# Kernel tuning notes

Hardware: AMD Instinct MI355X
Metric: run time of the kernel (lower is better)

Reference implementation:

```python
import jax, jax.numpy as jnp
import numpy as np

B, D, H, HD, P, O, K = 256, 1024, 8, 128, 2048, 1024, 4
HID = H * HD
EPS = 1e-5


def setup_inputs() -> dict:
    key = jax.random.key(0)
    ks = jax.random.split(key, 16)

    def w(k, shape, fan_in):
        return jax.random.normal(k, shape, jnp.float32) / np.sqrt(fan_in).astype(np.float32)

    return dict(
        seq=jax.random.normal(ks[0], (B, D), jnp.float32),
        c_tm1=jnp.zeros((B, H, HD, HD), jnp.float32),
        n_tm1=jnp.ones((B, H, HD), jnp.float32),
        m_tm1=jnp.zeros((B, H), jnp.float32),
        ln_g=jnp.ones((D,), jnp.float32), ln_b=jnp.zeros((D,), jnp.float32),
        gn_g=jnp.ones((HID,), jnp.float32), gn_b=jnp.zeros((HID,), jnp.float32),
        W_upl=w(ks[1], (P, D), D), b_upl=jnp.zeros((P,), jnp.float32),
        W_upr=w(ks[2], (HID, D), D), b_upr=jnp.zeros((HID,), jnp.float32),
        W_down=w(ks[3], (D, HID), HID), b_down=jnp.zeros((D,), jnp.float32),
        W_last=w(ks[4], (O, D), D), b_last=jnp.zeros((O,), jnp.float32),
        conv_w=w(ks[5], (K,), K), conv_b=jnp.zeros((), jnp.float32),
        W_skip=w(ks[6], (HID, P), P),
        W_i=w(ks[7], (H, P), P), b_i=jnp.zeros((H,), jnp.float32),
        W_f=w(ks[8], (H, P), P), b_f=jnp.zeros((H,), jnp.float32),
        W_o=w(ks[9], (HID, P), P), b_o=jnp.zeros((HID,), jnp.float32),
        W_q=w(ks[10], (HID, P), P), b_q=jnp.zeros((HID,), jnp.float32),
        W_k=w(ks[11], (HID, P), P), b_k=jnp.zeros((HID,), jnp.float32),
        W_v=w(ks[12], (HID, P), P), b_v=jnp.zeros((HID,), jnp.float32),
    )


def reference(seq, c_tm1, n_tm1, m_tm1, ln_g, ln_b, gn_g, gn_b,
              W_upl, b_upl, W_upr, b_upr, W_down, b_down, W_last, b_last,
              conv_w, conv_b, W_skip, W_i, b_i, W_f, b_f, W_o, b_o,
              W_q, b_q, W_k, b_k, W_v, b_v):
    b = seq.shape[0]
    h, hd = c_tm1.shape[1], c_tm1.shape[2]

    # input LayerNorm
    mu = jnp.mean(seq, -1, keepdims=True)
    var = jnp.var(seq, -1, keepdims=True)
    x_n = (seq - mu) * jax.lax.rsqrt(var + EPS) * ln_g + ln_b

    x_t = x_n @ W_upl.T + b_upl            # [b, P]
    r_t = x_n @ W_upr.T + b_upr            # [b, HID]

    # causal conv over the feature axis (in=out=1 channel), left pad K-1
    k_sz = conv_w.shape[0]
    p = x_t.shape[1]
    xp = jnp.pad(x_t, ((0, 0), (k_sz - 1, 0)))
    x_c = conv_b + sum(conv_w[j] * xp[:, j:j + p] for j in range(k_sz))
    x_c = jax.nn.silu(x_c)                 # [b, P]

    q_t = (x_c @ W_q.T + b_q).reshape(b, h, hd)
    k_t = ((x_c @ W_k.T + b_k) / np.sqrt(hd).astype(np.float32)).reshape(b, h, hd)
    v_t = (x_t @ W_v.T + b_v).reshape(b, h, hd)

    i_t = x_c @ W_i.T + b_i                # [b, h]
    f_t = x_c @ W_f.T + b_f                # [b, h]
    o_t = jax.nn.sigmoid(x_t @ W_o.T + b_o)  # [b, HID]

    # stabilized exponential gating
    m_t = jnp.maximum(f_t + m_tm1, i_t)
    i_g = jnp.exp(i_t - m_t)
    f_g = jnp.exp(f_t - m_t + m_tm1)

    # matrix-memory covariance update
    c_t = f_g[:, :, None, None] * c_tm1 + i_g[:, :, None, None] * jnp.einsum('bhd,bhp->bhdp', v_t, k_t)
    n_t = f_g[:, :, None] * n_tm1 + i_g[:, :, None] * k_t

    num = jnp.einsum('bhdp,bhp->bhd', c_t, q_t)
    den = jnp.maximum(jnp.einsum('bhd,bhd->bh', n_t, q_t), 1.0)
    h_t = o_t * (num / den[:, :, None]).reshape(b, h * hd)

    # GroupNorm(head_num groups) over hidden
    hg = h_t.reshape(b, h, hd)
    gmu = jnp.mean(hg, -1, keepdims=True)
    gvar = jnp.var(hg, -1, keepdims=True)
    hn = ((hg - gmu) * jax.lax.rsqrt(gvar + EPS)).reshape(b, h * hd) * gn_g + gn_b

    out = hn + x_c @ W_skip.T              # 1x1 conv skip == matmul
    out = out * jax.nn.silu(r_t)
    out = out @ W_down.T + b_down
    final = (out + x_n) @ W_last.T + b_last
    return final, c_t, n_t, m_t
```

## Files before the change

### kernel.cpp

```cpp
#include <hip/hip_runtime.h>
#include <cstdint>
#include <cstddef>

#define LN_EPS 1e-5f

typedef float  f32x4  __attribute__((ext_vector_type(4)));
typedef __bf16 bf16x8 __attribute__((ext_vector_type(8)));
typedef unsigned short u16x4 __attribute__((ext_vector_type(4)));

__global__ __launch_bounds__(256)
void k_ln(const float* __restrict__ seq, const float* __restrict__ g,
          const float* __restrict__ b, float* __restrict__ xn) {
  __shared__ float red[8];
  const int row = blockIdx.x, t = threadIdx.x;
  const f32x4 x = ((const f32x4*)(seq + (size_t)row * 1024))[t];
  float s  = x[0] + x[1] + x[2] + x[3];
  float s2 = x[0]*x[0] + x[1]*x[1] + x[2]*x[2] + x[3]*x[3];
#pragma unroll
  for (int o = 32; o > 0; o >>= 1) { s += __shfl_down(s, o, 64); s2 += __shfl_down(s2, o, 64); }
  const int lane = t & 63, w = t >> 6;
  if (lane == 0) { red[w] = s; red[4 + w] = s2; }
  __syncthreads();
  s  = red[0] + red[1] + red[2] + red[3];
  s2 = red[4] + red[5] + red[6] + red[7];
  const float mu  = s * (1.f / 1024.f);
  const float inv = rsqrtf(s2 * (1.f / 1024.f) - mu * mu + LN_EPS);
  const f32x4 gg = ((const f32x4*)g)[t];
  const f32x4 bb = ((const f32x4*)b)[t];
  f32x4 y;
#pragma unroll
  for (int i = 0; i < 4; ++i) y[i] = (x[i] - mu) * inv * gg[i] + bb[i];
  ((f32x4*)(xn + (size_t)row * 1024))[t] = y;
}

__global__ __launch_bounds__(256)
void k_conv(const float* __restrict__ xt, const float* __restrict__ cw,
            const float* __restrict__ cb, float* __restrict__ xc) {
  __shared__ float s[2048];
  const int row = blockIdx.x, t = threadIdx.x;
  const f32x4* src = (const f32x4*)(xt + (size_t)row * 2048);
  ((f32x4*)s)[t] = src[t];
  ((f32x4*)s)[t + 256] = src[t + 256];
  const float w0 = cw[0], w1 = cw[1], w2 = cw[2], w3 = cw[3], b = cb[0];
  __syncthreads();
  float out[8];
  const int c0 = t * 8;
#pragma unroll
  for (int j = 0; j < 8; ++j) {
    const int c = c0 + j;
    float a = b + w3 * s[c];
    if (c >= 1) a += w2 * s[c - 1];
    if (c >= 2) a += w1 * s[c - 2];
    if (c >= 3) a += w0 * s[c - 3];
    a = a / (1.f + __expf(-a));
    out[j] = a;
  }
  f32x4* dst = (f32x4*)(xc + (size_t)row * 2048 + c0);
  f32x4 v0 = {out[0], out[1], out[2], out[3]};
  f32x4 v1 = {out[4], out[5], out[6], out[7]};
  dst[0] = v0; dst[1] = v1;
}

__global__ __launch_bounds__(256)
void k_if(const float* __restrict__ xc, const float* __restrict__ Wi,
          const float* __restrict__ bi, const float* __restrict__ Wf,
          const float* __restrict__ bfp, const float* __restrict__ m_tm1,
          float* __restrict__ m_out, float* __restrict__ ig, float* __restrict__ fg) {
  __shared__ float sx[2048];
  __shared__ float so[16];
  const int row = blockIdx.x, t = threadIdx.x;
  const f32x4* src = (const f32x4*)(xc + (size_t)row * 2048);
  ((f32x4*)sx)[t] = src[t];
  ((f32x4*)sx)[t + 256] = src[t + 256];
  __syncthreads();
  const int w = t >> 6, lane = t & 63;
  float p[4];
#pragma unroll
  for (int i = 0; i < 4; ++i) {
    const int o = w * 4 + i;
    const float* wr = (o < 8) ? (Wi + (size_t)o * 2048) : (Wf + (size_t)(o - 8) * 2048);
    float acc = 0.f;
#pragma unroll
    for (int j = 0; j < 8; ++j) {
      const f32x4 xv = ((const f32x4*)sx)[j * 64 + lane];
      const f32x4 wv = ((const f32x4*)wr)[j * 64 + lane];
      acc += xv[0]*wv[0] + xv[1]*wv[1] + xv[2]*wv[2] + xv[3]*wv[3];
    }
    p[i] = acc;
  }
#pragma unroll
  for (int i = 0; i < 4; ++i) {
#pragma unroll
    for (int o = 32; o > 0; o >>= 1) p[i] += __shfl_xor(p[i], o, 64);
  }
  if (lane == 0) {
#pragma unroll
    for (int i = 0; i < 4; ++i) so[w * 4 + i] = p[i];
  }
  __syncthreads();
  if (t < 8) {
    const float it = so[t] + bi[t];
    const float ft = so[t + 8] + bfp[t];
    const float mp = m_tm1[row * 8 + t];
    const float m = fmaxf(ft + mp, it);
    m_out[row * 8 + t] = m;
    ig[row * 8 + t] = __expf(it - m);
    fg[row * 8 + t] = __expf(ft - m + mp);
  }
}

__global__ __launch_bounds__(256)
void k_rec_stream(const float* __restrict__ c_tm1, const float* __restrict__ kb,
                  const float* __restrict__ qb, const float* __restrict__ vb,
                  const float* __restrict__ ig, const float* __restrict__ fg,
                  float* __restrict__ c_out, float* __restrict__ numG) {
  const int blk = blockIdx.x;
  const int bh = blk >> 2;
  const int rg = blk & 3;
  const int t = threadIdx.x;
  const int w = t >> 6, lane = t & 63;
  const int c4 = lane & 31;
  const int half = lane >> 5;
  const int b = bh >> 3, h = bh & 7;
  const size_t vecbase = (size_t)b * 1024 + h * 128;
  const float fgv = fg[bh], igv = ig[bh];
  const f32x4 k4 = ((const f32x4*)(kb + vecbase))[c4];
  const f32x4 q4 = ((const f32x4*)(qb + vecbase))[c4];
  const int row0 = rg * 32 + w * 8;
  const f32x4* C0 = (const f32x4*)(c_tm1 + (size_t)bh * 16384);
  f32x4* Ct = (f32x4*)(c_out + (size_t)bh * 16384);
  f32x4 c0s[4]; float vrow[4];
#pragma unroll
  for (int j = 0; j < 4; ++j) {
    const int r = row0 + 2 * j + half;
    c0s[j] = C0[r * 32 + c4];
    vrow[j] = vb[vecbase + r];
  }
#pragma unroll
  for (int j = 0; j < 4; ++j)
    asm volatile("" : "+v"(c0s[j][0]), "+v"(c0s[j][1]), "+v"(c0s[j][2]), "+v"(c0s[j][3]));
  float pd[4];
#pragma unroll
  for (int j = 0; j < 4; ++j) {
    const int r = row0 + 2 * j + half;
    const float iv = igv * vrow[j];
    f32x4 ct = fgv * c0s[j] + iv * k4;
    Ct[r * 32 + c4] = ct;
    pd[j] = ct[0] * q4[0] + ct[1] * q4[1] + ct[2] * q4[2] + ct[3] * q4[3];
  }
#pragma unroll
  for (int j = 0; j < 4; ++j) {
    float p = pd[j];
    p += __shfl_xor(p, 1, 64); p += __shfl_xor(p, 2, 64); p += __shfl_xor(p, 4, 64);
    p += __shfl_xor(p, 8, 64); p += __shfl_xor(p, 16, 64);
    if (c4 == 0) numG[(size_t)bh * 128 + row0 + 2 * j + half] = p;
  }
}

__device__ __forceinline__ float bsum128(float v, volatile float* red) {
#pragma unroll
  for (int o = 32; o > 0; o >>= 1) v += __shfl_xor(v, o, 64);
  const int w = threadIdx.x >> 6;
  __syncthreads();
  if ((threadIdx.x & 63) == 0) red[w] = v;
  __syncthreads();
  return red[0] + red[1];
}

__global__ __launch_bounds__(128)
void k_rec_fin(const float* __restrict__ n_tm1, const float* __restrict__ kb,
               const float* __restrict__ qb, const float* __restrict__ ot,
               const float* __restrict__ ig, const float* __restrict__ fg,
               const float* __restrict__ numG,
               const float* __restrict__ gn_g, const float* __restrict__ gn_b,
               const float* __restrict__ skipb, const float* __restrict__ sr,
               float* __restrict__ n_out, float* __restrict__ uf) {
  __shared__ float red[2];
  const int bh = blockIdx.x, t = threadIdx.x;
  const int b = bh >> 3, h = bh & 7;
  const size_t base = (size_t)b * 1024 + h * 128;
  const float fgv = fg[bh], igv = ig[bh];
  const float ntd = fgv * n_tm1[(size_t)bh * 128 + t] + igv * kb[base + t];
  n_out[(size_t)bh * 128 + t] = ntd;
  const float den = fmaxf(bsum128(ntd * qb[base + t], red), 1.f);
  const float o = 1.f / (1.f + __expf(-ot[base + t]));
  const float hv = o * numG[(size_t)bh * 128 + t] / den;
  const float mu  = bsum128(hv, red) * (1.f / 128.f);
  const float var = bsum128(hv * hv, red) * (1.f / 128.f) - mu * mu;
  const int hid = h * 128 + t;
  const float hn = (hv - mu) * rsqrtf(var + LN_EPS) * gn_g[hid] + gn_b[hid];
  uf[base + t] = (hn + skipb[base + t]) * sr[base + t];
}

struct GemmSeg {
  const float* A; const float* W; const float* bias; float* out;
  const float* add; int ldOut; int colOfs; int epi; float scale;
};
struct GemmArgs { GemmSeg seg[5]; };

__global__ __launch_bounds__(256)
void k_gemm(int K, GemmArgs ga) {
  __shared__ __align__(16) char lds[32768];
  const int tid = threadIdx.x;
  const int lane = tid & 63;
  const int wid = tid >> 6;
  const int wm = wid >> 1;
  const int wn = wid & 1;
  const int segId = blockIdx.x >> 4;
  const int n0 = (blockIdx.x & 15) * 64;
  const int m0 = blockIdx.y * 64;
  const GemmSeg sg = ga.seg[segId];

  const int lrow = tid >> 4;
  const int col4 = tid & 15;

  f32x4 acc[2][2] = {};

  const float* Abase = sg.A + (size_t)m0 * K;
  const float* Wbase = sg.W + (size_t)n0 * K;
  const int NT = K >> 6;

  f32x4 va[4], vw[4], va2[4], vw2[4];
#pragma unroll
  for (int p = 0; p < 4; ++p) {
    const int r = p * 16 + lrow;
    va[p] = *(const f32x4*)(Abase + (size_t)r * K + col4 * 4);
    vw[p] = *(const f32x4*)(Wbase + (size_t)r * K + col4 * 4);
  }

  for (int kt = 0; kt < NT; ++kt) {
    __syncthreads();
    {
      const int byte = ((((col4 >> 1) ^ (lrow & 7)) << 4) | ((col4 & 1) << 3));
#pragma unroll
      for (int p = 0; p < 4; ++p) {
        const int r = p * 16 + lrow;
        u16x4 ah, al, wh, wl;
#pragma unroll
        for (int i = 0; i < 4; ++i) {
          const unsigned ab = __float_as_uint(va[p][i]);
          const float fh = __uint_as_float(ab & 0xFFFF0000u);
          ah[i] = (unsigned short)(ab >> 16);
          al[i] = (unsigned short)(__float_as_uint(va[p][i] - fh) >> 16);
          const unsigned wb2 = __float_as_uint(vw[p][i]);
          const float wfh = __uint_as_float(wb2 & 0xFFFF0000u);
          wh[i] = (unsigned short)(wb2 >> 16);
          wl[i] = (unsigned short)(__float_as_uint(vw[p][i] - wfh) >> 16);
        }
        *(u16x4*)(lds + r * 128 + byte) = ah;
        *(u16x4*)(lds + 8192 + r * 128 + byte) = al;
        *(u16x4*)(lds + 16384 + r * 128 + byte) = wh;
        *(u16x4*)(lds + 24576 + r * 128 + byte) = wl;
      }
    }
    if (kt + 1 < NT) {
      const int ko = (kt + 1) * 64;
#pragma unroll
      for (int p = 0; p < 4; ++p) {
        const int r = p * 16 + lrow;
        va2[p] = *(const f32x4*)(Abase + (size_t)r * K + ko + col4 * 4);
        vw2[p] = *(const f32x4*)(Wbase + (size_t)r * K + ko + col4 * 4);
      }
    }
    __syncthreads();
    {
      const int rA = wm * 32 + (lane & 15);
      const int rB = wn * 32 + (lane & 15);
      const int kg = lane >> 4;
      const int swz = lane & 7;
#pragma unroll
      for (int kk = 0; kk < 2; ++kk) {
        const int so = ((kk * 4 + kg) ^ swz) << 4;
        const char* pa0 = lds + rA * 128 + so;
        const char* pa1 = lds + (rA + 16) * 128 + so;
        const char* pb0 = lds + 16384 + rB * 128 + so;
        const char* pb1 = lds + 16384 + (rB + 16) * 128 + so;
        const bf16x8 ah0 = *(const bf16x8*)(pa0);
        const bf16x8 al0 = *(const bf16x8*)(pa0 + 8192);
        const bf16x8 ah1 = *(const bf16x8*)(pa1);
        const bf16x8 al1 = *(const bf16x8*)(pa1 + 8192);
        const bf16x8 bh0 = *(const bf16x8*)(pb0);
        const bf16x8 bl0 = *(const bf16x8*)(pb0 + 8192);
        const bf16x8 bh1 = *(const bf16x8*)(pb1);
        const bf16x8 bl1 = *(const bf16x8*)(pb1 + 8192);
        acc[0][0] = __builtin_amdgcn_mfma_f32_16x16x32_bf16(ah0, bh0, acc[0][0], 0, 0, 0);
        acc[0][1] = __builtin_amdgcn_mfma_f32_16x16x32_bf16(ah0, bh1, acc[0][1], 0, 0, 0);
        acc[1][0] = __builtin_amdgcn_mfma_f32_16x16x32_bf16(ah1, bh0, acc[1][0], 0, 0, 0);
        acc[1][1] = __builtin_amdgcn_mfma_f32_16x16x32_bf16(ah1, bh1, acc[1][1], 0, 0, 0);
        acc[0][0] = __builtin_amdgcn_mfma_f32_16x16x32_bf16(ah0, bl0, acc[0][0], 0, 0, 0);
        acc[0][1] = __builtin_amdgcn_mfma_f32_16x16x32_bf16(ah0, bl1, acc[0][1], 0, 0, 0);
        acc[1][0] = __builtin_amdgcn_mfma_f32_16x16x32_bf16(ah1, bl0, acc[1][0], 0, 0, 0);
        acc[1][1] = __builtin_amdgcn_mfma_f32_16x16x32_bf16(ah1, bl1, acc[1][1], 0, 0, 0);
        acc[0][0] = __builtin_amdgcn_mfma_f32_16x16x32_bf16(al0, bh0, acc[0][0], 0, 0, 0);
        acc[0][1] = __builtin_amdgcn_mfma_f32_16x16x32_bf16(al0, bh1, acc[0][1], 0, 0, 0);
        acc[1][0] = __builtin_amdgcn_mfma_f32_16x16x32_bf16(al1, bh0, acc[1][0], 0, 0, 0);
        acc[1][1] = __builtin_amdgcn_mfma_f32_16x16x32_bf16(al1, bh1, acc[1][1], 0, 0, 0);
      }
    }
#pragma unroll
    for (int p = 0; p < 4; ++p) { va[p] = va2[p]; vw[p] = vw2[p]; }
  }

  const int rowb = m0 + wm * 32 + (lane >> 4) * 4;
  const int colb = n0 + wn * 32 + (lane & 15);
#pragma unroll
  for (int mf = 0; mf < 2; ++mf) {
#pragma unroll
    for (int nf = 0; nf < 2; ++nf) {
      const int col = colb + nf * 16;
      const float bv = sg.bias ? sg.bias[col] : 0.f;
#pragma unroll
      for (int i = 0; i < 4; ++i) {
        const int row = rowb + mf * 16 + i;
        float v = acc[mf][nf][i] + bv;
        if (sg.epi == 1)      v = v / (1.f + __expf(-v));
        else if (sg.epi == 3) v *= sg.scale;
        else if (sg.epi == 4) v += sg.add[(size_t)row * 1024 + col];
        sg.out[(size_t)row * sg.ldOut + sg.colOfs + col] = v;
      }
    }
  }
}

extern "C" void kernel_launch(void* const* d_in, const int* in_sizes, int n_in,
                              void* d_out, int out_size, void* d_ws, size_t ws_size,
                              hipStream_t stream) {
  (void)in_sizes; (void)n_in; (void)out_size; (void)ws_size;
  const float* seq    = (const float*)d_in[0];
  const float* c_tm1  = (const float*)d_in[1];
  const float* n_tm1  = (const float*)d_in[2];
  const float* m_tm1  = (const float*)d_in[3];
  const float* ln_g   = (const float*)d_in[4];
  const float* ln_b   = (const float*)d_in[5];
  const float* gn_g   = (const float*)d_in[6];
  const float* gn_b   = (const float*)d_in[7];
  const float* W_upl  = (const float*)d_in[8];
  const float* b_upl  = (const float*)d_in[9];
  const float* W_upr  = (const float*)d_in[10];
  const float* b_upr  = (const float*)d_in[11];
  const float* W_down = (const float*)d_in[12];
  const float* b_down = (const float*)d_in[13];
  const float* W_last = (const float*)d_in[14];
  const float* b_last = (const float*)d_in[15];
  const float* conv_w = (const float*)d_in[16];
  const float* conv_b = (const float*)d_in[17];
  const float* W_skip = (const float*)d_in[18];
  const float* W_i    = (const float*)d_in[19];
  const float* b_i    = (const float*)d_in[20];
  const float* W_f    = (const float*)d_in[21];
  const float* b_f    = (const float*)d_in[22];
  const float* W_o    = (const float*)d_in[23];
  const float* b_o    = (const float*)d_in[24];
  const float* W_q    = (const float*)d_in[25];
  const float* b_q    = (const float*)d_in[26];
  const float* W_k    = (const float*)d_in[27];
  const float* b_k    = (const float*)d_in[28];
  const float* W_v    = (const float*)d_in[29];
  const float* b_v    = (const float*)d_in[30];

  float* out_final = (float*)d_out;
  float* out_c = out_final + (size_t)256 * 1024;
  float* out_n = out_c + (size_t)256 * 8 * 128 * 128;
  float* out_m = out_n + (size_t)256 * 8 * 128;

  char* ws = (char*)d_ws;
  size_t off = 0;
  auto alloc = [&](size_t bytes) -> void* {
    void* p = ws + off; off += (bytes + 255) & ~(size_t)255; return p;
  };
  float* x_n   = (float*)alloc((size_t)256 * 1024 * 4);
  float* x_t   = (float*)alloc((size_t)256 * 2048 * 4);
  float* sr    = (float*)alloc((size_t)256 * 1024 * 4);
  float* x_c   = (float*)alloc((size_t)256 * 2048 * 4);
  float* qb    = (float*)alloc((size_t)256 * 1024 * 4);
  float* kb    = (float*)alloc((size_t)256 * 1024 * 4);
  float* vb    = (float*)alloc((size_t)256 * 1024 * 4);
  float* otb   = (float*)alloc((size_t)256 * 1024 * 4);
  float* skipb = (float*)alloc((size_t)256 * 1024 * 4);
  float* igb   = (float*)alloc((size_t)2048 * 4);
  float* fgb   = (float*)alloc((size_t)2048 * 4);
  float* u_f   = (float*)alloc((size_t)256 * 1024 * 4);
  float* t_f   = (float*)alloc((size_t)256 * 1024 * 4);
  float* numG  = (float*)alloc((size_t)2048 * 128 * 4);

  k_ln<<<256, 256, 0, stream>>>(seq, ln_g, ln_b, x_n);

  GemmArgs gA = {};
  gA.seg[0] = {x_n, W_upl, b_upl, x_t, nullptr, 2048, 0, 0, 0.f};
  gA.seg[1] = {x_n, W_upl + (size_t)1024 * 1024, b_upl + 1024, x_t, nullptr, 2048, 1024, 0, 0.f};
  gA.seg[2] = {x_n, W_upr, b_upr, sr, nullptr, 1024, 0, 1, 0.f};
  k_gemm<<<dim3(48, 4), 256, 0, stream>>>(1024, gA);

  k_conv<<<256, 256, 0, stream>>>(x_t, conv_w, conv_b, x_c);

  k_if<<<256, 256, 0, stream>>>(x_c, W_i, b_i, W_f, b_f, m_tm1, out_m, igb, fgb);

  GemmArgs gBC = {};
  gBC.seg[0] = {x_c, W_q, b_q, qb, nullptr, 1024, 0, 0, 0.f};
  gBC.seg[1] = {x_c, W_k, b_k, kb, nullptr, 1024, 0, 3, 0.08838834764831845f};
  gBC.seg[2] = {x_c, W_skip, nullptr, skipb, nullptr, 1024, 0, 0, 0.f};
  gBC.seg[3] = {x_t, W_v, b_v, vb, nullptr, 1024, 0, 0, 0.f};
  gBC.seg[4] = {x_t, W_o, b_o, otb, nullptr, 1024, 0, 0, 0.f};
  k_gemm<<<dim3(80, 4), 256, 0, stream>>>(2048, gBC);

  k_rec_stream<<<8192, 256, 0, stream>>>(c_tm1, kb, qb, vb, igb, fgb, out_c, numG);

  k_rec_fin<<<2048, 128, 0, stream>>>(n_tm1, kb, qb, otb, igb, fgb, numG,
                                      gn_g, gn_b, skipb, sr, out_n, u_f);

  GemmArgs gD = {};
  gD.seg[0] = {u_f, W_down, b_down, t_f, x_n, 1024, 0, 4, 0.f};
  k_gemm<<<dim3(16, 4), 256, 0, stream>>>(1024, gD);

  GemmArgs gE = {};
  gE.seg[0] = {t_f, W_last, b_last, out_final, nullptr, 1024, 0, 0, 0.f};
  k_gemm<<<dim3(16, 4), 256, 0, stream>>>(1024, gE);
}
```

Measured before the change: 189.0 us.

## Split recurrence into separate numerator and covariance-update kernels using algebraic decomposition

```diff
diff --git a/kernel.cpp b/kernel.cpp
--- a/kernel.cpp
+++ b/kernel.cpp
@@ -110,10 +110,41 @@
 }
 
 __global__ __launch_bounds__(256)
-void k_rec_stream(const float* __restrict__ c_tm1, const float* __restrict__ kb,
-                  const float* __restrict__ qb, const float* __restrict__ vb,
-                  const float* __restrict__ ig, const float* __restrict__ fg,
-                  float* __restrict__ c_out, float* __restrict__ numG) {
+void k_num(const float* __restrict__ c_tm1, const float* __restrict__ qb,
+           float* __restrict__ rawG) {
+  const int blk = blockIdx.x;
+  const int bh = blk >> 2;
+  const int rg = blk & 3;
+  const int t = threadIdx.x;
+  const int w = t >> 6, lane = t & 63;
+  const int c4 = lane & 31;
+  const int half = lane >> 5;
+  const int b = bh >> 3, h = bh & 7;
+  const size_t vecbase = (size_t)b * 1024 + h * 128;
+  const f32x4 q4 = ((const f32x4*)(qb + vecbase))[c4];
+  const int row0 = rg * 32 + w * 8;
+  const f32x4* C0 = (const f32x4*)(c_tm1 + (size_t)bh * 16384);
+  f32x4 c0s[4];
+#pragma unroll
+  for (int j = 0; j < 4; ++j)
+    c0s[j] = C0[(row0 + 2 * j + half) * 32 + c4];
+  float pd[4];
+#pragma unroll
+  for (int j = 0; j < 4; ++j)
+    pd[j] = c0s[j][0] * q4[0] + c0s[j][1] * q4[1] + c0s[j][2] * q4[2] + c0s[j][3] * q4[3];
+#pragma unroll
+  for (int j = 0; j < 4; ++j) {
+    float p = pd[j];
+    p += __shfl_xor(p, 1, 64); p += __shfl_xor(p, 2, 64); p += __shfl_xor(p, 4, 64);
+    p += __shfl_xor(p, 8, 64); p += __shfl_xor(p, 16, 64);
+    if (c4 == 0) rawG[(size_t)bh * 128 + row0 + 2 * j + half] = p;
+  }
+}
+
+__global__ __launch_bounds__(256)
+void k_ct(const float* __restrict__ c_tm1, const float* __restrict__ kb,
+          const float* __restrict__ vb, const float* __restrict__ ig,
+          const float* __restrict__ fg, float* __restrict__ c_out) {
   const int blk = blockIdx.x;
   const int bh = blk >> 2;
   const int rg = blk & 3;
@@ -125,7 +156,6 @@
   const size_t vecbase = (size_t)b * 1024 + h * 128;
   const float fgv = fg[bh], igv = ig[bh];
   const f32x4 k4 = ((const f32x4*)(kb + vecbase))[c4];
-  const f32x4 q4 = ((const f32x4*)(qb + vecbase))[c4];
   const int row0 = rg * 32 + w * 8;
   const f32x4* C0 = (const f32x4*)(c_tm1 + (size_t)bh * 16384);
   f32x4* Ct = (f32x4*)(c_out + (size_t)bh * 16384);
@@ -136,24 +166,12 @@
     c0s[j] = C0[r * 32 + c4];
     vrow[j] = vb[vecbase + r];
   }
-#pragma unroll
-  for (int j = 0; j < 4; ++j)
-    asm volatile("" : "+v"(c0s[j][0]), "+v"(c0s[j][1]), "+v"(c0s[j][2]), "+v"(c0s[j][3]));
-  float pd[4];
 #pragma unroll
   for (int j = 0; j < 4; ++j) {
     const int r = row0 + 2 * j + half;
     const float iv = igv * vrow[j];
     f32x4 ct = fgv * c0s[j] + iv * k4;
     Ct[r * 32 + c4] = ct;
-    pd[j] = ct[0] * q4[0] + ct[1] * q4[1] + ct[2] * q4[2] + ct[3] * q4[3];
-  }
-#pragma unroll
-  for (int j = 0; j < 4; ++j) {
-    float p = pd[j];
-    p += __shfl_xor(p, 1, 64); p += __shfl_xor(p, 2, 64); p += __shfl_xor(p, 4, 64);
-    p += __shfl_xor(p, 8, 64); p += __shfl_xor(p, 16, 64);
-    if (c4 == 0) numG[(size_t)bh * 128 + row0 + 2 * j + half] = p;
   }
 }
 
@@ -169,9 +187,10 @@
 
 __global__ __launch_bounds__(128)
 void k_rec_fin(const float* __restrict__ n_tm1, const float* __restrict__ kb,
-               const float* __restrict__ qb, const float* __restrict__ ot,
+               const float* __restrict__ qb, const float* __restrict__ vb,
+               const float* __restrict__ ot,
                const float* __restrict__ ig, const float* __restrict__ fg,
-               const float* __restrict__ numG,
+               const float* __restrict__ rawG,
                const float* __restrict__ gn_g, const float* __restrict__ gn_b,
                const float* __restrict__ skipb, const float* __restrict__ sr,
                float* __restrict__ n_out, float* __restrict__ uf) {
@@ -180,11 +199,14 @@
   const int b = bh >> 3, h = bh & 7;
   const size_t base = (size_t)b * 1024 + h * 128;
   const float fgv = fg[bh], igv = ig[bh];
-  const float ntd = fgv * n_tm1[(size_t)bh * 128 + t] + igv * kb[base + t];
+  const float kv = kb[base + t], qv = qb[base + t];
+  const float kq = bsum128(kv * qv, red);
+  const float num = fgv * rawG[(size_t)bh * 128 + t] + igv * kq * vb[base + t];
+  const float ntd = fgv * n_tm1[(size_t)bh * 128 + t] + igv * kv;
   n_out[(size_t)bh * 128 + t] = ntd;
-  const float den = fmaxf(bsum128(ntd * qb[base + t], red), 1.f);
+  const float den = fmaxf(bsum128(ntd * qv, red), 1.f);
   const float o = 1.f / (1.f + __expf(-ot[base + t]));
-  const float hv = o * numG[(size_t)bh * 128 + t] / den;
+  const float hv = o * num / den;
   const float mu  = bsum128(hv, red) * (1.f / 128.f);
   const float var = bsum128(hv * hv, red) * (1.f / 128.f) - mu * mu;
   const int hid = h * 128 + t;
@@ -381,7 +403,7 @@
   float* fgb   = (float*)alloc((size_t)2048 * 4);
   float* u_f   = (float*)alloc((size_t)256 * 1024 * 4);
   float* t_f   = (float*)alloc((size_t)256 * 1024 * 4);
-  float* numG  = (float*)alloc((size_t)2048 * 128 * 4);
+  float* rawG  = (float*)alloc((size_t)2048 * 128 * 4);
 
   k_ln<<<256, 256, 0, stream>>>(seq, ln_g, ln_b, x_n);
 
@@ -403,9 +425,11 @@
   gBC.seg[4] = {x_t, W_o, b_o, otb, nullptr, 1024, 0, 0, 0.f};
   k_gemm<<<dim3(80, 4), 256, 0, stream>>>(2048, gBC);
 
-  k_rec_stream<<<8192, 256, 0, stream>>>(c_tm1, kb, qb, vb, igb, fgb, out_c, numG);
-
-  k_rec_fin<<<2048, 128, 0, stream>>>(n_tm1, kb, qb, otb, igb, fgb, numG,
+  k_num<<<8192, 256, 0, stream>>>(c_tm1, qb, rawG);
+
+  k_ct<<<8192, 256, 0, stream>>>(c_tm1, kb, vb, igb, fgb, out_c);
+
+  k_rec_fin<<<2048, 128, 0, stream>>>(n_tm1, kb, qb, vb, otb, igb, fgb, rawG,
                                       gn_g, gn_b, skipb, sr, out_n, u_f);
 
   GemmArgs gD = {};
```

After: 209.6 us. 1.11x slower.
